# Kernel optimization log

Measured on AMD Instinct MI355X. Metric: run time of the kernel, lower is better.

Reference implementation:

```python
import jax, jax.numpy as jnp
import numpy as np

# NOTE: the original source omits the definitions of QSVT, quantum_lcu_block,
# QuantumSumBlock and KANLayer. We reconstruct the standard math these blocks
# implement in quantum-KAN papers/repos:
#   QSVT(x)            -> vector of Chebyshev polynomials T_1..T_D of the
#                         (squashed) input, the polynomial basis QSVT realizes.
#   quantum_lcu_block  -> linear combination of unitaries: weighted sum of the
#                         QSVT vector normalized by the LCU l1 weight norm.
#   QuantumSumBlock    -> learnable interference sum: mean_k sin(alpha_k * v).
#   KANLayer           -> Chebyshev-KAN layer: spline term (Chebyshev basis
#                         contracted with coeffs) + SiLU base branch + bias.
# Everything is fully vectorized over (B, F) instead of the original per-scalar
# Python loops.

B, F, DEG, C, KBASIS = 16384, 512, 8, 10, 8


def _cheb(x, K):
    """Chebyshev features T_1..T_K of x in (-1, 1): shape x.shape + (K,)."""
    t = jnp.arccos(jnp.clip(x, -1.0, 1.0))
    k = jnp.arange(1, K + 1, dtype=x.dtype)
    return jnp.cos(t[..., None] * k)


def setup_inputs() -> dict:
    key = jax.random.key(0)
    ks = jax.random.split(key, 6)
    return {
        "X": jax.random.normal(ks[0], (B, F), dtype=jnp.float32),
        # nn.Parameter(torch.rand(num_features, degree))
        "lcu_weights": jax.random.uniform(ks[1], (F, DEG), dtype=jnp.float32),
        # one QuantumSumBlock(degree) per feature -> (F, DEG) phases
        "sum_alpha": jax.random.normal(ks[2], (F, DEG), dtype=jnp.float32),
        # KANLayer params
        "kan_coeff": jax.random.normal(ks[3], (C, F, KBASIS), dtype=jnp.float32) * 0.1,
        "kan_base": jax.random.normal(ks[4], (C, F), dtype=jnp.float32) * 0.1,
        "kan_bias": jnp.zeros((C,), dtype=jnp.float32),
    }


def reference(X, lcu_weights, sum_alpha, kan_coeff, kan_base, kan_bias):
    # squash inputs into the open interval (-1, 1) for the Chebyshev/QSVT basis
    x = 0.99 * jnp.tanh(X)                                   # (B, F)
    # QSVT polynomial feature vector per scalar, batched: (B, F, DEG)
    qsvt = _cheb(x, lcu_weights.shape[1])
    # LCU block: weighted combination normalized by l1 norm of weights -> (B, F)
    lcu = jnp.einsum('bfd,fd->bf', qsvt, lcu_weights) / (
        jnp.sum(jnp.abs(lcu_weights), axis=-1) + 1e-8)
    # Quantum sum block: learnable sinusoidal interference sum -> (B, F)
    summed = jnp.mean(jnp.sin(lcu[..., None] * sum_alpha), axis=-1)
    # Chebyshev-KAN layer
    s = 0.99 * jnp.tanh(summed)
    phi = _cheb(s, kan_coeff.shape[2])                       # (B, F, KBASIS)
    logits = (jnp.einsum('bfk,cfk->bc', phi, kan_coeff)
              + jax.nn.silu(summed) @ kan_base.T
              + kan_bias)                                    # (B, C)
    return logits
```

## Files before the change

### kernel.cpp

```cpp
#include <hip/hip_runtime.h>
#include <hip/hip_bf16.h>

#define BATCH 16384
#define NF    512
#define DEG   8
#define NC    10
#define KB    8

#define RB    16
#define PITCH (NF + 4)
#define NT    256

#define CBN (NC * NF * KB)
#define BBN (NC * NF)

#define INV2PI 0.15915494309189535f
#define LOG2E  1.4426950408889634f

typedef __attribute__((ext_vector_type(2))) float v2f;
typedef __attribute__((ext_vector_type(8))) short bfrag;
typedef __attribute__((ext_vector_type(4))) float f32x4;

union frag_u { bfrag s; unsigned u[4]; };

__device__ __forceinline__ v2f v2fma(v2f a, v2f b, v2f c) {
    return __builtin_elementwise_fma(a, b, c);
}
__device__ __forceinline__ v2f v2exp(v2f x) {
    v2f a = x * LOG2E;
    v2f r; r.x = __builtin_amdgcn_exp2f(a.x); r.y = __builtin_amdgcn_exp2f(a.y);
    return r;
}
__device__ __forceinline__ v2f v2rcp(v2f x) {
    v2f r; r.x = __builtin_amdgcn_rcpf(x.x); r.y = __builtin_amdgcn_rcpf(x.y);
    return r;
}
__device__ __forceinline__ v2f v2sin2pi(v2f x) {
    v2f r; r.x = __builtin_amdgcn_sinf(x.x); r.y = __builtin_amdgcn_sinf(x.y);
    return r;
}
__device__ __forceinline__ v2f v2tanh99(v2f x) {
    v2f e = v2exp(x + x);
    v2f r = v2rcp(e + 1.0f);
    return v2fma(r, (v2f)(-1.98f), (v2f)(0.99f));
}
__device__ __forceinline__ v2f v2silu(v2f v) {
    v2f e = v2exp(-v);
    v2f r = v2rcp(e + 1.0f);
    return v * r;
}
__device__ __forceinline__ unsigned cvtpk2(float lo, float hi) {
    __hip_bfloat162 h = __float22bfloat162_rn(float2{lo, hi});
    unsigned u;
    __builtin_memcpy(&u, &h, sizeof(u));
    return u;
}

__global__ __launch_bounds__(256) void prep_kernel(
    const float* __restrict__ coeff, const float* __restrict__ base,
    unsigned short* __restrict__ pk)
{
    const int i = blockIdx.x * 256 + threadIdx.x;
    if (i < CBN)
        pk[i] = (unsigned short)((__builtin_bit_cast(unsigned, coeff[i]) + 0x8000u) >> 16);
    else if (i < CBN + BBN)
        pk[i] = (unsigned short)((__builtin_bit_cast(unsigned, base[i - CBN]) + 0x8000u) >> 16);
}

__global__ __launch_bounds__(NT, 4) void qkan_kernel(
    const float* __restrict__ X,
    const float* __restrict__ lcu_w,
    const float* __restrict__ alpha,
    const unsigned short* __restrict__ pk,
    const float* __restrict__ bias,
    float* __restrict__ out)
{
    __shared__ float s_mem[RB * PITCH];
    __shared__ float s_red[4 * RB * 16];

    const int t    = threadIdx.x;
    const int row0 = blockIdx.x * RB;

    {
        const int fA = t * 2;

        float wa[2][DEG], aa[2][DEG], den[2];
#pragma unroll
        for (int i = 0; i < 2; ++i) {
            const float4 w0 = *(const float4*)(lcu_w + (fA + i) * DEG);
            const float4 w1 = *(const float4*)(lcu_w + (fA + i) * DEG + 4);
            const float4 a0 = *(const float4*)(alpha + (fA + i) * DEG);
            const float4 a1 = *(const float4*)(alpha + (fA + i) * DEG + 4);
            wa[i][0]=w0.x; wa[i][1]=w0.y; wa[i][2]=w0.z; wa[i][3]=w0.w;
            wa[i][4]=w1.x; wa[i][5]=w1.y; wa[i][6]=w1.z; wa[i][7]=w1.w;
            aa[i][0]=a0.x; aa[i][1]=a0.y; aa[i][2]=a0.z; aa[i][3]=a0.w;
            aa[i][4]=a1.x; aa[i][5]=a1.y; aa[i][6]=a1.z; aa[i][7]=a1.w;
            float d = 1e-8f;
#pragma unroll
            for (int k = 0; k < DEG; ++k) d += fabsf(wa[i][k]);
            den[i] = d;
        }
        v2f W[DEG], A2[DEG];
#pragma unroll
        for (int d = 0; d < DEG; ++d) {
            W[d]  = (v2f){wa[0][d], wa[1][d]};
            A2[d] = (v2f){aa[0][d] * INV2PI, aa[1][d] * INV2PI};
        }
        const v2f rden = (v2f){__builtin_amdgcn_rcpf(den[0]),
                               __builtin_amdgcn_rcpf(den[1])};

#pragma unroll 4
        for (int r = 0; r < RB; ++r) {
            const v2f xv = *(const v2f*)(X + (row0 + r) * NF + fA);
            const v2f x  = v2tanh99(xv);
            const v2f x2 = x + x;
            v2f tkm1 = (v2f){1.0f, 1.0f}, tk = x, num = (v2f){0.0f, 0.0f};
#pragma unroll
            for (int d = 0; d < DEG; ++d) {
                num = v2fma(W[d], tk, num);
                v2f tn = v2fma(x2, tk, -tkm1);
                tkm1 = tk; tk = tn;
            }
            const v2f lcu = num * rden;
            v2f ss = (v2f){0.0f, 0.0f};
#pragma unroll
            for (int d = 0; d < DEG; ++d)
                ss += v2sin2pi(lcu * A2[d]);
            *(v2f*)(&s_mem[r * PITCH + fA]) = ss * 0.125f;
        }
    }
    __syncthreads();

    const int lane = t & 63;
    const int wave = __builtin_amdgcn_readfirstlane(t >> 6);
    const int n    = lane & 15;
    const int q    = lane >> 4;
    const int ncl  = (n < NC) ? n : (NC - 1);
    const int fw   = wave * 128;

    const unsigned short* cb = pk;
    const unsigned short* bb = pk + CBN;
    const unsigned short* cbase = cb + (ncl * NF + fw) * KB;

    f32x4 acc0 = {0.f, 0.f, 0.f, 0.f};
    f32x4 acc1 = {0.f, 0.f, 0.f, 0.f};

#pragma unroll 4
    for (int kp = 0; kp < 16; ++kp) {
        const bfrag b0 = *(const bfrag*)(cbase + (kp * 8 + q) * KB);
        const bfrag b1 = *(const bfrag*)(cbase + (kp * 8 + 4 + q) * KB);

        const float sA = s_mem[n * PITCH + fw + kp * 8 + q];
        const float sB = s_mem[n * PITCH + fw + kp * 8 + 4 + q];
        const v2f s  = v2tanh99((v2f){sA, sB});
        const v2f s2 = s + s;
        v2f T[KB];
        {
            v2f tkm1 = (v2f){1.0f, 1.0f}, tk = s;
#pragma unroll
            for (int k = 0; k < KB; ++k) {
                T[k] = tk;
                v2f tn = v2fma(s2, tk, -tkm1);
                tkm1 = tk; tk = tn;
            }
        }
        frag_u fa0, fa1;
#pragma unroll
        for (int i = 0; i < 4; ++i) {
            fa0.u[i] = cvtpk2(T[2 * i].x, T[2 * i + 1].x);
            fa1.u[i] = cvtpk2(T[2 * i].y, T[2 * i + 1].y);
        }
        acc0 = __builtin_amdgcn_mfma_f32_16x16x32_bf16(fa0.s, b0, acc0, 0, 0, 0);
        acc1 = __builtin_amdgcn_mfma_f32_16x16x32_bf16(fa1.s, b1, acc1, 0, 0, 0);
    }

#pragma unroll
    for (int kt2 = 0; kt2 < 4; ++kt2) {
        const bfrag b = *(const bfrag*)(bb + ncl * NF + fw + kt2 * 32 + q * 8);
        const int off = n * PITCH + fw + kt2 * 32 + q * 8;
        const float4 v0 = *(const float4*)(&s_mem[off]);
        const float4 v1 = *(const float4*)(&s_mem[off + 4]);
        v2f vv[4] = {{v0.x, v0.y}, {v0.z, v0.w}, {v1.x, v1.y}, {v1.z, v1.w}};
        frag_u fa;
#pragma unroll
        for (int g = 0; g < 4; ++g) {
            const v2f sl = v2silu(vv[g]);
            fa.u[g] = cvtpk2(sl.x, sl.y);
        }
        if (kt2 & 1)
            acc1 = __builtin_amdgcn_mfma_f32_16x16x32_bf16(fa.s, b, acc1, 0, 0, 0);
        else
            acc0 = __builtin_amdgcn_mfma_f32_16x16x32_bf16(fa.s, b, acc0, 0, 0, 0);
    }

    const f32x4 acc = acc0 + acc1;
#pragma unroll
    for (int i = 0; i < 4; ++i)
        s_red[(wave * RB + q * 4 + i) * 16 + n] = acc[i];
    __syncthreads();

    if (t < RB * NC) {
        const int r = t / NC;
        const int c = t - r * NC;
        float v = bias[c];
#pragma unroll
        for (int w = 0; w < 4; ++w)
            v += s_red[(w * RB + r) * 16 + c];
        out[(row0 + r) * NC + c] = v;
    }
}

extern "C" void kernel_launch(void* const* d_in, const int* in_sizes, int n_in,
                              void* d_out, int out_size, void* d_ws, size_t ws_size,
                              hipStream_t stream) {
    const float* X      = (const float*)d_in[0];
    const float* lcu_w  = (const float*)d_in[1];
    const float* alpha  = (const float*)d_in[2];
    const float* coeff  = (const float*)d_in[3];
    const float* base   = (const float*)d_in[4];
    const float* bias   = (const float*)d_in[5];
    float* out = (float*)d_out;
    unsigned short* pk = (unsigned short*)d_ws;

    prep_kernel<<<(CBN + BBN + 255) / 256, 256, 0, stream>>>(coeff, base, pk);
    qkan_kernel<<<BATCH / RB, NT, 0, stream>>>(X, lcu_w, alpha, pk, bias, out);
}
```

Measured before the change: 99.84 us.

## Double threads per block to 8 waves and store intermediates as bf16 in LDS

Grows the block from 256 to 512 threads. Each half of the block now computes the quantum-sum stage for 8 of the 16 rows, and each of the 8 waves runs the KAN MFMA stage over 64 features instead of 128. The shared intermediate is stored as bf16 rather than fp32, which halves LDS use, and the cross-wave reduction is widened to 8 waves. The aim is more parallelism per block, shorter per-wave dependent loops and a smaller LDS footprint. The cost is an extra bf16 rounding of the sum value before its tanh, plus a longer final reduction.

```diff
diff --git a/kernel.cpp b/kernel.cpp
--- a/kernel.cpp
+++ b/kernel.cpp
@@ -7,9 +7,10 @@
 #define NC    10
 #define KB    8
 
-#define RB    16
-#define PITCH (NF + 4)
-#define NT    256
+#define RB     16
+#define PITCH2 520
+#define NT     512
+#define NWAVES 8
 
 #define CBN (NC * NF * KB)
 #define BBN (NC * NF)
@@ -19,6 +20,7 @@
 
 typedef __attribute__((ext_vector_type(2))) float v2f;
 typedef __attribute__((ext_vector_type(8))) short bfrag;
+typedef __attribute__((ext_vector_type(8))) unsigned short us8;
 typedef __attribute__((ext_vector_type(4))) float f32x4;
 
 union frag_u { bfrag s; unsigned u[4]; };
@@ -54,6 +56,10 @@
     unsigned u;
     __builtin_memcpy(&u, &h, sizeof(u));
     return u;
+}
+__device__ __forceinline__ float bf2f(unsigned short h) {
+    unsigned u = ((unsigned)h) << 16;
+    return __builtin_bit_cast(float, u);
 }
 
 __global__ __launch_bounds__(256) void prep_kernel(
@@ -67,7 +73,7 @@
         pk[i] = (unsigned short)((__builtin_bit_cast(unsigned, base[i - CBN]) + 0x8000u) >> 16);
 }
 
-__global__ __launch_bounds__(NT, 4) void qkan_kernel(
+__global__ __launch_bounds__(NT, 8) void qkan_kernel(
     const float* __restrict__ X,
     const float* __restrict__ lcu_w,
     const float* __restrict__ alpha,
@@ -75,14 +81,15 @@
     const float* __restrict__ bias,
     float* __restrict__ out)
 {
-    __shared__ float s_mem[RB * PITCH];
-    __shared__ float s_red[4 * RB * 16];
+    __shared__ unsigned short s_mem[RB * PITCH2];
+    __shared__ float s_red[NWAVES * RB * 16];
 
     const int t    = threadIdx.x;
     const int row0 = blockIdx.x * RB;
 
     {
-        const int fA = t * 2;
+        const int fA = (t & 255) * 2;
+        const int rh = (t >> 8) * 8;
 
         float wa[2][DEG], aa[2][DEG], den[2];
 #pragma unroll
@@ -110,7 +117,8 @@
                                __builtin_amdgcn_rcpf(den[1])};
 
 #pragma unroll 4
-        for (int r = 0; r < RB; ++r) {
+        for (int r8 = 0; r8 < 8; ++r8) {
+            const int r = rh + r8;
             const v2f xv = *(const v2f*)(X + (row0 + r) * NF + fA);
             const v2f x  = v2tanh99(xv);
             const v2f x2 = x + x;
@@ -126,7 +134,8 @@
 #pragma unroll
             for (int d = 0; d < DEG; ++d)
                 ss += v2sin2pi(lcu * A2[d]);
-            *(v2f*)(&s_mem[r * PITCH + fA]) = ss * 0.125f;
+            const v2f sm = ss * 0.125f;
+            *(unsigned*)(&s_mem[r * PITCH2 + fA]) = cvtpk2(sm.x, sm.y);
         }
     }
     __syncthreads();
@@ -136,7 +145,7 @@
     const int n    = lane & 15;
     const int q    = lane >> 4;
     const int ncl  = (n < NC) ? n : (NC - 1);
-    const int fw   = wave * 128;
+    const int fw   = wave * 64;
 
     const unsigned short* cb = pk;
     const unsigned short* bb = pk + CBN;
@@ -146,12 +155,12 @@
     f32x4 acc1 = {0.f, 0.f, 0.f, 0.f};
 
 #pragma unroll 4
-    for (int kp = 0; kp < 16; ++kp) {
+    for (int kp = 0; kp < 8; ++kp) {
         const bfrag b0 = *(const bfrag*)(cbase + (kp * 8 + q) * KB);
         const bfrag b1 = *(const bfrag*)(cbase + (kp * 8 + 4 + q) * KB);
 
-        const float sA = s_mem[n * PITCH + fw + kp * 8 + q];
-        const float sB = s_mem[n * PITCH + fw + kp * 8 + 4 + q];
+        const float sA = bf2f(s_mem[n * PITCH2 + fw + kp * 8 + q]);
+        const float sB = bf2f(s_mem[n * PITCH2 + fw + kp * 8 + 4 + q]);
         const v2f s  = v2tanh99((v2f){sA, sB});
         const v2f s2 = s + s;
         v2f T[KB];
@@ -175,12 +184,13 @@
     }
 
 #pragma unroll
-    for (int kt2 = 0; kt2 < 4; ++kt2) {
+    for (int kt2 = 0; kt2 < 2; ++kt2) {
         const bfrag b = *(const bfrag*)(bb + ncl * NF + fw + kt2 * 32 + q * 8);
-        const int off = n * PITCH + fw + kt2 * 32 + q * 8;
-        const float4 v0 = *(const float4*)(&s_mem[off]);
-        const float4 v1 = *(const float4*)(&s_mem[off + 4]);
-        v2f vv[4] = {{v0.x, v0.y}, {v0.z, v0.w}, {v1.x, v1.y}, {v1.z, v1.w}};
+        const us8 sv = *(const us8*)(&s_mem[n * PITCH2 + fw + kt2 * 32 + q * 8]);
+        v2f vv[4];
+#pragma unroll
+        for (int g = 0; g < 4; ++g)
+            vv[g] = (v2f){bf2f(sv[2 * g]), bf2f(sv[2 * g + 1])};
         frag_u fa;
 #pragma unroll
         for (int g = 0; g < 4; ++g) {
@@ -196,7 +206,7 @@
     const f32x4 acc = acc0 + acc1;
 #pragma unroll
     for (int i = 0; i < 4; ++i)
-        s_red[(wave * RB + q * 4 + i) * 16 + n] = acc[i];
+        s_red[wave * (RB * 16) + (q * 4 + i) * 16 + n] = acc[i];
     __syncthreads();
 
     if (t < RB * NC) {
@@ -204,8 +214,8 @@
         const int c = t - r * NC;
         float v = bias[c];
 #pragma unroll
-        for (int w = 0; w < 4; ++w)
-            v += s_red[(w * RB + r) * 16 + c];
+        for (int w = 0; w < NWAVES; ++w)
+            v += s_red[w * (RB * 16) + r * 16 + c];
         out[(row0 + r) * NC + c] = v;
     }
 }
```

Result: no change. 101.6 us (+1.8%).
